# Kernel tuning notes

Hardware: AMD Instinct MI355X
Metric: run time of the kernel (lower is better)

The kernel has to match this reference:

```python
import jax, jax.numpy as jnp
import numpy as np

D_MODEL = 1024
NUM_HEADS = 16
HEAD_DIM = D_MODEL // NUM_HEADS


def setup_inputs() -> dict:
    key = jax.random.key(0)
    ks = jax.random.split(key, 10)
    B, L = 2, 2048
    s = 1.0 / np.sqrt(D_MODEL)
    x = jax.random.normal(ks[0], (B, L, D_MODEL), dtype=jnp.float32)
    Wq = jax.random.normal(ks[1], (D_MODEL, D_MODEL), dtype=jnp.float32) * s
    bq = jnp.zeros((D_MODEL,), dtype=jnp.float32)
    Wk = jax.random.normal(ks[2], (D_MODEL, D_MODEL), dtype=jnp.float32) * s
    bk = jnp.zeros((D_MODEL,), dtype=jnp.float32)
    Wv = jax.random.normal(ks[3], (D_MODEL, D_MODEL), dtype=jnp.float32) * s
    bv = jnp.zeros((D_MODEL,), dtype=jnp.float32)
    Wo = jax.random.normal(ks[4], (D_MODEL, D_MODEL), dtype=jnp.float32) * s
    bo = jnp.zeros((D_MODEL,), dtype=jnp.float32)
    # per-head retention decay; torch init is ones, use values near 1 for nontrivial decay
    gamma = jax.random.uniform(ks[5], (NUM_HEADS,), dtype=jnp.float32, minval=0.95, maxval=1.0)
    return {"x": x, "Wq": Wq, "bq": bq, "Wk": Wk, "bk": bk,
            "Wv": Wv, "bv": bv, "Wo": Wo, "bo": bo, "gamma": gamma}


def reference(x, Wq, bq, Wk, bk, Wv, bv, Wo, bo, gamma):
    B, L, D = x.shape
    H, hd = NUM_HEADS, HEAD_DIM
    # projections (torch Linear: x @ W.T + b), split heads -> [B, H, L, hd]
    q = (x @ Wq.T + bq).reshape(B, L, H, hd).transpose(0, 2, 1, 3)
    k = (x @ Wk.T + bk).reshape(B, L, H, hd).transpose(0, 2, 1, 3)
    v = (x @ Wv.T + bv).reshape(B, L, H, hd).transpose(0, 2, 1, 3)
    # per-head decay gamma_h^i applied along the query index (matches torch broadcast)
    idx = jnp.arange(L, dtype=x.dtype)
    decay = gamma[None, :, None, None] ** idx[None, None, :, None]  # [1, H, L, 1]
    scores = jnp.einsum('bhqd,bhkd->bhqk', q, k)  # [B, H, L, L]
    causal = jnp.tril(jnp.ones((L, L), dtype=x.dtype))
    scores = scores * causal[None, None] * decay
    out = jnp.einsum('bhqk,bhkd->bhqd', scores, v)  # [B, H, L, hd]
    out = out.transpose(0, 2, 1, 3).reshape(B, L, D)
    return out @ Wo.T + bo
```

## Files before the change

### kernel.cpp

```cpp
#include <hip/hip_runtime.h>
#include <hip/hip_bf16.h>

#define D_MODEL 1024
#define NUM_HEADS 16
#define HEAD_DIM 64
#define BATCH 2
#define SEQ 2048
#define M_TOT (BATCH*SEQ)
#define CHUNK 64
#define NCHUNK (SEQ/CHUNK)
#define LT 68

typedef __attribute__((ext_vector_type(8))) short bf16x8;
typedef __attribute__((ext_vector_type(8))) unsigned short us16x8;
typedef __attribute__((ext_vector_type(4))) float f32x4;

__device__ inline ushort f2bf(float f) {
    __hip_bfloat16 h = __float2bfloat16(f);
    return __builtin_bit_cast(ushort, h);
}

__device__ inline bf16x8 ld_frag(const ushort* p) {
    struct S { uint2 a, b; };
    S s;
    s.a = *(const uint2*)p;
    s.b = *(const uint2*)(p + 4);
    return __builtin_bit_cast(bf16x8, s);
}

__device__ inline void st16(ushort* dst, uint4 a, uint4 b) {
    *(uint2*)(dst + 0)  = make_uint2(a.x, a.y);
    *(uint2*)(dst + 4)  = make_uint2(a.z, a.w);
    *(uint2*)(dst + 8)  = make_uint2(b.x, b.y);
    *(uint2*)(dst + 12) = make_uint2(b.z, b.w);
}

__device__ inline void load_lds16(const ushort* g, ushort* l) {
    __builtin_amdgcn_global_load_lds(
        (const __attribute__((address_space(1))) unsigned int*)g,
        (__attribute__((address_space(3))) unsigned int*)l, 16, 0, 0);
}

#define XN (M_TOT * D_MODEL)
#define WN (D_MODEL * D_MODEL)
__global__ __launch_bounds__(256) void cast_all_kernel(const float* __restrict__ x,
                                                       const float* __restrict__ Wq,
                                                       const float* __restrict__ Wk,
                                                       const float* __restrict__ Wv,
                                                       const float* __restrict__ Wo,
                                                       ushort* __restrict__ dst) {
    size_t o = ((size_t)blockIdx.x * 256 + threadIdx.x) * 4;
    const float* src;
    if (o < XN)               src = x  + o;
    else if (o < XN + WN)     src = Wq + (o - XN);
    else if (o < XN + 2 * WN) src = Wk + (o - XN - WN);
    else if (o < XN + 3 * WN) src = Wv + (o - XN - 2 * (size_t)WN);
    else                      src = Wo + (o - XN - 3 * (size_t)WN);
    float4 f = *(const float4*)src;
    ushort4 u;
    u.x = f2bf(f.x); u.y = f2bf(f.y); u.z = f2bf(f.z); u.w = f2bf(f.w);
    *(ushort4*)(dst + o) = u;
}

__global__ __launch_bounds__(256) void decay_kernel(const float* __restrict__ gamma,
                                                    float* __restrict__ decay) {
    int idx = blockIdx.x * blockDim.x + threadIdx.x;
    if (idx < SEQ * NUM_HEADS) {
        int i = idx >> 4, h = idx & 15;
        decay[idx] = powf(gamma[h], (float)i);
    }
}

template <int NBUF, int OUT_BF16>
__global__ __launch_bounds__(256) void gemm128(const ushort* __restrict__ A,
                                               const ushort* __restrict__ Bt,
                                               const float* __restrict__ b0,
                                               const float* __restrict__ b1,
                                               const float* __restrict__ b2,
                                               void* __restrict__ o0,
                                               void* __restrict__ o1,
                                               void* __restrict__ o2,
                                               const float* __restrict__ decay) {
    const int K = 1024;
    __shared__ ushort lds_a[128 * 64];
    __shared__ ushort lds_b[128 * 64];
    int t = threadIdx.x;
    int lane = t & 63, w = t >> 6;
    int bm = blockIdx.y * 128, bn = blockIdx.x * 128;
    int wm = (w >> 1) * 64, wn = (w & 1) * 64;

    int lr = lane >> 3, lc = lane & 7;
    int gcol = lc ^ (lr & 7);
    const ushort* aBase = A  + (size_t)(bm + w * 32 + lr) * K + gcol * 8;
    const ushort* bBase = Bt + (size_t)(bn + w * 32 + lr) * K + gcol * 8;
    ushort* aLds = &lds_a[(w * 32) * 64];
    ushort* bLds = &lds_b[(w * 32) * 64];

    f32x4 acc[4][4];
    #pragma unroll
    for (int i = 0; i < 4; i++)
        #pragma unroll
        for (int j = 0; j < 4; j++)
            acc[i][j] = (f32x4){0.f, 0.f, 0.f, 0.f};

    int mrel = lane & 15, kq = lane >> 4;

    for (int k0 = 0; k0 < K; k0 += 64) {
        #pragma unroll
        for (int q = 0; q < 4; q++) {
            load_lds16(aBase + (size_t)q * 8 * K + k0, aLds + q * 512);
            load_lds16(bBase + (size_t)q * 8 * K + k0, bLds + q * 512);
        }
        __syncthreads();
        #pragma unroll
        for (int s = 0; s < 2; s++) {
            bf16x8 af[4], bfv[4];
            #pragma unroll
            for (int i = 0; i < 4; i++) {
                int row = wm + i * 16 + mrel;
                af[i] = ld_frag(&lds_a[row * 64 + (((s * 4 + kq) ^ (row & 7)) * 8)]);
            }
            #pragma unroll
            for (int j = 0; j < 4; j++) {
                int row = wn + j * 16 + mrel;
                bfv[j] = ld_frag(&lds_b[row * 64 + (((s * 4 + kq) ^ (row & 7)) * 8)]);
            }
            #pragma unroll
            for (int i = 0; i < 4; i++)
                #pragma unroll
                for (int j = 0; j < 4; j++)
                    acc[i][j] = __builtin_amdgcn_mfma_f32_16x16x32_bf16(af[i], bfv[j], acc[i][j], 0, 0, 0);
        }
        __syncthreads();
    }

    int quad = lane >> 4;
    int buf = (NBUF == 3) ? (bn >> 10) : 0;
    const float* bias = (buf == 0) ? b0 : (buf == 1) ? b1 : b2;
    void* dstv = (buf == 0) ? o0 : (buf == 1) ? o1 : o2;
    int cbase = ((NBUF == 3) ? (bn & 1023) : bn) + wn;
    #pragma unroll
    for (int j = 0; j < 4; j++) {
        int cl = cbase + j * 16 + mrel;
        float bv = bias[cl];
        #pragma unroll
        for (int i = 0; i < 4; i++) {
            #pragma unroll
            for (int reg = 0; reg < 4; reg++) {
                int row = bm + wm + i * 16 + quad * 4 + reg;
                float v = acc[i][j][reg] + bv;
                if (NBUF == 3 && buf == 0)
                    v *= decay[(row & (SEQ - 1)) * 16 + (cl >> 6)];
                if (OUT_BF16)
                    ((ushort*)dstv)[(size_t)row * 1024 + cl] = f2bf(v);
                else
                    ((float*)dstv)[(size_t)row * 1024 + cl] = v;
            }
        }
    }
}

__global__ __launch_bounds__(256) void chunk_kv_mfma(const ushort* __restrict__ kp,
                                                     const ushort* __restrict__ vp,
                                                     float* __restrict__ states) {
    __shared__ ushort Kt[64 * LT];
    __shared__ ushort Vt[64 * LT];
    int bx = blockIdx.x;
    int c = bx & 31, h = (bx >> 5) & 15, b = bx >> 9;
    int t = threadIdx.x, lane = t & 63, w = t >> 6;
    size_t rowbase = (size_t)(b * SEQ + c * 64);
    int r = t >> 2, cc = t & 3;
    const uint4* gk = (const uint4*)(kp + (rowbase + r) * D_MODEL + h * 64 + cc * 16);
    const uint4* gv = (const uint4*)(vp + (rowbase + r) * D_MODEL + h * 64 + cc * 16);
    uint4 k0 = gk[0], k1 = gk[1], v0 = gv[0], v1 = gv[1];
    {
        us16x8 ka = __builtin_bit_cast(us16x8, k0), kb = __builtin_bit_cast(us16x8, k1);
        us16x8 va = __builtin_bit_cast(us16x8, v0), vb = __builtin_bit_cast(us16x8, v1);
        #pragma unroll
        for (int i = 0; i < 8; i++) {
            Kt[(cc * 16 + i) * LT + r]     = ka[i];
            Kt[(cc * 16 + 8 + i) * LT + r] = kb[i];
            Vt[(cc * 16 + i) * LT + r]     = va[i];
            Vt[(cc * 16 + 8 + i) * LT + r] = vb[i];
        }
    }
    __syncthreads();
    int mrel = lane & 15, q8 = (lane >> 4) * 8, band = w * 16;
    bf16x8 af[2];
    af[0] = ld_frag(&Vt[(band + mrel) * LT + q8]);
    af[1] = ld_frag(&Vt[(band + mrel) * LT + 32 + q8]);
    f32x4 acc[4];
    #pragma unroll
    for (int dt = 0; dt < 4; dt++) acc[dt] = (f32x4){0.f, 0.f, 0.f, 0.f};
    #pragma unroll
    for (int dt = 0; dt < 4; dt++)
        #pragma unroll
        for (int kk = 0; kk < 2; kk++)
            acc[dt] = __builtin_amdgcn_mfma_f32_16x16x32_bf16(
                af[kk], ld_frag(&Kt[(dt * 16 + mrel) * LT + kk * 32 + q8]), acc[dt], 0, 0, 0);
    int quad = lane >> 4;
    float* sp = states + (size_t)bx * 4096;
    #pragma unroll
    for (int dt = 0; dt < 4; dt++)
        #pragma unroll
        for (int reg = 0; reg < 4; reg++)
            sp[(band + quad * 4 + reg) * 64 + dt * 16 + mrel] = acc[dt][reg];
}

__global__ __launch_bounds__(256) void prefix_kernel(const float* __restrict__ states,
                                                     ushort* __restrict__ statesb) {
    int bh = blockIdx.y;
    int e = blockIdx.x * 256 + threadIdx.x;
    const float* src = states + (size_t)bh * NCHUNK * 4096 + e;
    ushort* dst = statesb + (size_t)bh * NCHUNK * 4096 + e;
    float run = 0.f;
    for (int cb = 0; cb < NCHUNK; cb += 8) {
        float vals[8];
        #pragma unroll
        for (int u = 0; u < 8; u++) vals[u] = src[(size_t)(cb + u) * 4096];
        #pragma unroll
        for (int u = 0; u < 8; u++) {
            dst[(size_t)(cb + u) * 4096] = f2bf(run);
            run += vals[u];
        }
    }
}

__global__ __launch_bounds__(256) void attn_mfma(const ushort* __restrict__ qp,
                                                 const ushort* __restrict__ kp,
                                                 const ushort* __restrict__ vp,
                                                 const ushort* __restrict__ statesb,
                                                 ushort* __restrict__ attn_out) {
    __shared__ ushort Qs[64 * LT];
    __shared__ ushort Ks[64 * LT];
    __shared__ ushort Vt[64 * LT];
    __shared__ ushort St[64 * LT];
    __shared__ ushort Ps[64 * LT];
    int bx = blockIdx.x;
    int c = bx & 31, h = (bx >> 5) & 15, b = bx >> 9;
    int t = threadIdx.x, lane = t & 63, w = t >> 6;
    size_t rowbase = (size_t)(b * SEQ + c * 64);
    int r = t >> 2, cc = t & 3;
    {
        const uint4* gq = (const uint4*)(qp + (rowbase + r) * D_MODEL + h * 64 + cc * 16);
        const uint4* gk = (const uint4*)(kp + (rowbase + r) * D_MODEL + h * 64 + cc * 16);
        const uint4* gv = (const uint4*)(vp + (rowbase + r) * D_MODEL + h * 64 + cc * 16);
        const uint4* gs = (const uint4*)(statesb + (size_t)bx * 4096 + t * 16);
        uint4 q0 = gq[0], q1 = gq[1];
        uint4 k0 = gk[0], k1 = gk[1];
        uint4 v0 = gv[0], v1 = gv[1];
        uint4 s0 = gs[0], s1 = gs[1];
        st16(&Qs[r * LT + cc * 16], q0, q1);
        st16(&Ks[r * LT + cc * 16], k0, k1);
        st16(&St[r * LT + cc * 16], s0, s1);
        us16x8 va = __builtin_bit_cast(us16x8, v0), vb = __builtin_bit_cast(us16x8, v1);
        #pragma unroll
        for (int i = 0; i < 8; i++) {
            Vt[(cc * 16 + i) * LT + r]     = va[i];
            Vt[(cc * 16 + 8 + i) * LT + r] = vb[i];
        }
    }
    __syncthreads();

    int mrel = lane & 15, q8 = (lane >> 4) * 8, quad = lane >> 4, band = w * 16;
    bf16x8 af[2];
    af[0] = ld_frag(&Qs[(band + mrel) * LT + q8]);
    af[1] = ld_frag(&Qs[(band + mrel) * LT + 32 + q8]);

    f32x4 oacc[4];
    #pragma unroll
    for (int dt = 0; dt < 4; dt++) oacc[dt] = (f32x4){0.f, 0.f, 0.f, 0.f};
    #pragma unroll
    for (int dt = 0; dt < 4; dt++)
        #pragma unroll
        for (int kk = 0; kk < 2; kk++)
            oacc[dt] = __builtin_amdgcn_mfma_f32_16x16x32_bf16(
                af[kk], ld_frag(&St[(dt * 16 + mrel) * LT + kk * 32 + q8]), oacc[dt], 0, 0, 0);

    f32x4 pacc[4];
    #pragma unroll
    for (int jt = 0; jt < 4; jt++) pacc[jt] = (f32x4){0.f, 0.f, 0.f, 0.f};
    #pragma unroll
    for (int jt = 0; jt < 4; jt++) {
        if (jt <= w) {
            #pragma unroll
            for (int kk = 0; kk < 2; kk++)
                pacc[jt] = __builtin_amdgcn_mfma_f32_16x16x32_bf16(
                    af[kk], ld_frag(&Ks[(jt * 16 + mrel) * LT + kk * 32 + q8]), pacc[jt], 0, 0, 0);
        }
    }
    #pragma unroll
    for (int jt = 0; jt < 4; jt++) {
        #pragma unroll
        for (int reg = 0; reg < 4; reg++) {
            int i = band + quad * 4 + reg;
            int j = jt * 16 + mrel;
            float val = (jt <= w && j <= i) ? pacc[jt][reg] : 0.f;
            Ps[i * LT + j] = f2bf(val);
        }
    }
    __syncthreads();

    bf16x8 pf0 = ld_frag(&Ps[(band + mrel) * LT + q8]);
    #pragma unroll
    for (int dt = 0; dt < 4; dt++)
        oacc[dt] = __builtin_amdgcn_mfma_f32_16x16x32_bf16(
            pf0, ld_frag(&Vt[(dt * 16 + mrel) * LT + q8]), oacc[dt], 0, 0, 0);
    if (w >= 2) {
        bf16x8 pf1 = ld_frag(&Ps[(band + mrel) * LT + 32 + q8]);
        #pragma unroll
        for (int dt = 0; dt < 4; dt++)
            oacc[dt] = __builtin_amdgcn_mfma_f32_16x16x32_bf16(
                pf1, ld_frag(&Vt[(dt * 16 + mrel) * LT + 32 + q8]), oacc[dt], 0, 0, 0);
    }

    #pragma unroll
    for (int dt = 0; dt < 4; dt++) {
        #pragma unroll
        for (int reg = 0; reg < 4; reg++) {
            size_t row = rowbase + band + quad * 4 + reg;
            int col = h * 64 + dt * 16 + mrel;
            attn_out[row * D_MODEL + col] = f2bf(oacc[dt][reg]);
        }
    }
}

extern "C" void kernel_launch(void* const* d_in, const int* in_sizes, int n_in,
                              void* d_out, int out_size, void* d_ws, size_t ws_size,
                              hipStream_t stream) {
    (void)in_sizes; (void)n_in; (void)out_size; (void)ws_size;
    const float* x  = (const float*)d_in[0];
    const float* Wq = (const float*)d_in[1];
    const float* bq = (const float*)d_in[2];
    const float* Wk = (const float*)d_in[3];
    const float* bk = (const float*)d_in[4];
    const float* Wv = (const float*)d_in[5];
    const float* bv = (const float*)d_in[6];
    const float* Wo = (const float*)d_in[7];
    const float* bo = (const float*)d_in[8];
    const float* gamma = (const float*)d_in[9];
    float* out = (float*)d_out;

    uint8_t* w = (uint8_t*)d_ws;
    ushort* xb    = (ushort*)w; w += (size_t)XN * 2;
    ushort* wqkvb = (ushort*)w; w += (size_t)3 * WN * 2;
    ushort* wob   = (ushort*)w; w += (size_t)WN * 2;
    ushort* qb  = (ushort*)w; w += (size_t)XN * 2;
    ushort* kb  = (ushort*)w; w += (size_t)XN * 2;
    ushort* vb  = (ushort*)w; w += (size_t)XN * 2;
    float*  states  = (float*)w;  w += (size_t)BATCH * NUM_HEADS * NCHUNK * 4096 * 4;
    ushort* statesb = (ushort*)w; w += (size_t)BATCH * NUM_HEADS * NCHUNK * 4096 * 2;
    float*  decay   = (float*)w;  w += (size_t)SEQ * NUM_HEADS * 4;

    cast_all_kernel<<<(XN + 4 * WN) / 4 / 256, 256, 0, stream>>>(x, Wq, Wk, Wv, Wo, xb);
    decay_kernel<<<(SEQ * NUM_HEADS) / 256, 256, 0, stream>>>(gamma, decay);

    gemm128<3, 1><<<dim3(3072 / 128, M_TOT / 128), 256, 0, stream>>>(
        xb, wqkvb, bq, bk, bv, qb, kb, vb, decay);

    int nblk = BATCH * NUM_HEADS * NCHUNK;
    chunk_kv_mfma<<<nblk, 256, 0, stream>>>(kb, vb, states);
    prefix_kernel<<<dim3(16, 32), 256, 0, stream>>>(states, statesb);
    attn_mfma<<<nblk, 256, 0, stream>>>(qb, kb, vb, statesb, xb);

    gemm128<1, 0><<<dim3(1024 / 128, M_TOT / 128), 256, 0, stream>>>(
        xb, wob, bo, nullptr, nullptr, out, nullptr, nullptr, nullptr);
}
```

Measured before the change: 190.6 us.

## Fuse decay into cast kernel, remap GEMM blocks per XCD, store chunk states bf16

Computes the decay table inside the cast kernel using extra blocks, which removes one kernel launch. The GEMM block index is remapped so that blocks landing on the same XCD share columns of B, aiming for better L2 reuse. Chunk KV states are rounded to bf16 in LDS and written with coalesced 16-byte stores, and the prefix scan runs in place on the bf16 buffer, roughly halving state traffic. The in-place scan now sums values that were already rounded to bf16, so precision drops slightly.

```diff
diff --git a/kernel.cpp b/kernel.cpp
--- a/kernel.cpp
+++ b/kernel.cpp
@@ -19,6 +19,10 @@
     __hip_bfloat16 h = __float2bfloat16(f);
     return __builtin_bit_cast(ushort, h);
 }
+__device__ inline float bf2f(ushort u) {
+    unsigned int v = ((unsigned int)u) << 16;
+    return __builtin_bit_cast(float, v);
+}
 
 __device__ inline bf16x8 ld_frag(const ushort* p) {
     struct S { uint2 a, b; };
@@ -43,13 +47,23 @@
 
 #define XN (M_TOT * D_MODEL)
 #define WN (D_MODEL * D_MODEL)
+#define CAST_BLOCKS ((XN + 4 * WN) / 4 / 256)
 __global__ __launch_bounds__(256) void cast_all_kernel(const float* __restrict__ x,
                                                        const float* __restrict__ Wq,
                                                        const float* __restrict__ Wk,
                                                        const float* __restrict__ Wv,
                                                        const float* __restrict__ Wo,
-                                                       ushort* __restrict__ dst) {
-    size_t o = ((size_t)blockIdx.x * 256 + threadIdx.x) * 4;
+                                                       ushort* __restrict__ dst,
+                                                       const float* __restrict__ gamma,
+                                                       float* __restrict__ decay) {
+    int bx = blockIdx.x;
+    if (bx >= CAST_BLOCKS) {
+        int idx = (bx - CAST_BLOCKS) * 256 + threadIdx.x;
+        int i = idx >> 4, h = idx & 15;
+        decay[idx] = powf(gamma[h], (float)i);
+        return;
+    }
+    size_t o = ((size_t)bx * 256 + threadIdx.x) * 4;
     const float* src;
     if (o < XN)               src = x  + o;
     else if (o < XN + WN)     src = Wq + (o - XN);
@@ -60,15 +74,6 @@
     ushort4 u;
     u.x = f2bf(f.x); u.y = f2bf(f.y); u.z = f2bf(f.z); u.w = f2bf(f.w);
     *(ushort4*)(dst + o) = u;
-}
-
-__global__ __launch_bounds__(256) void decay_kernel(const float* __restrict__ gamma,
-                                                    float* __restrict__ decay) {
-    int idx = blockIdx.x * blockDim.x + threadIdx.x;
-    if (idx < SEQ * NUM_HEADS) {
-        int i = idx >> 4, h = idx & 15;
-        decay[idx] = powf(gamma[h], (float)i);
-    }
 }
 
 template <int NBUF, int OUT_BF16>
@@ -86,7 +91,12 @@
     __shared__ ushort lds_b[128 * 64];
     int t = threadIdx.x;
     int lane = t & 63, w = t >> 6;
-    int bm = blockIdx.y * 128, bn = blockIdx.x * 128;
+
+    int p = blockIdx.y * gridDim.x + blockIdx.x;
+    int xcd = p & 7, q = p >> 3;
+    int cpx = gridDim.x >> 3;
+    int bn = (xcd * cpx + (q % cpx)) * 128;
+    int bm = (q / cpx) * 128;
     int wm = (w >> 1) * 64, wn = (w & 1) * 64;
 
     int lr = lane >> 3, lc = lane & 7;
@@ -107,9 +117,9 @@
 
     for (int k0 = 0; k0 < K; k0 += 64) {
         #pragma unroll
-        for (int q = 0; q < 4; q++) {
-            load_lds16(aBase + (size_t)q * 8 * K + k0, aLds + q * 512);
-            load_lds16(bBase + (size_t)q * 8 * K + k0, bLds + q * 512);
+        for (int qq = 0; qq < 4; qq++) {
+            load_lds16(aBase + (size_t)qq * 8 * K + k0, aLds + qq * 512);
+            load_lds16(bBase + (size_t)qq * 8 * K + k0, bLds + qq * 512);
         }
         __syncthreads();
         #pragma unroll
@@ -162,7 +172,7 @@
 
 __global__ __launch_bounds__(256) void chunk_kv_mfma(const ushort* __restrict__ kp,
                                                      const ushort* __restrict__ vp,
-                                                     float* __restrict__ states) {
+                                                     ushort* __restrict__ statesb) {
     __shared__ ushort Kt[64 * LT];
     __shared__ ushort Vt[64 * LT];
     int bx = blockIdx.x;
@@ -185,7 +195,7 @@
         }
     }
     __syncthreads();
-    int mrel = lane & 15, q8 = (lane >> 4) * 8, band = w * 16;
+    int mrel = lane & 15, q8 = (lane >> 4) * 8, band = w * 16, quad = lane >> 4;
     bf16x8 af[2];
     af[0] = ld_frag(&Vt[(band + mrel) * LT + q8]);
     af[1] = ld_frag(&Vt[(band + mrel) * LT + 32 + q8]);
@@ -198,29 +208,34 @@
         for (int kk = 0; kk < 2; kk++)
             acc[dt] = __builtin_amdgcn_mfma_f32_16x16x32_bf16(
                 af[kk], ld_frag(&Kt[(dt * 16 + mrel) * LT + kk * 32 + q8]), acc[dt], 0, 0, 0);
-    int quad = lane >> 4;
-    float* sp = states + (size_t)bx * 4096;
+    __syncthreads();
     #pragma unroll
     for (int dt = 0; dt < 4; dt++)
         #pragma unroll
         for (int reg = 0; reg < 4; reg++)
-            sp[(band + quad * 4 + reg) * 64 + dt * 16 + mrel] = acc[dt][reg];
-}
-
-__global__ __launch_bounds__(256) void prefix_kernel(const float* __restrict__ states,
-                                                     ushort* __restrict__ statesb) {
+            Kt[(band + quad * 4 + reg) * LT + dt * 16 + mrel] = f2bf(acc[dt][reg]);
+    __syncthreads();
+    {
+        bf16x8 s0 = ld_frag(&Kt[r * LT + cc * 16]);
+        bf16x8 s1 = ld_frag(&Kt[r * LT + cc * 16 + 8]);
+        uint4* dst = (uint4*)(statesb + (size_t)bx * 4096 + r * 64 + cc * 16);
+        dst[0] = __builtin_bit_cast(uint4, s0);
+        dst[1] = __builtin_bit_cast(uint4, s1);
+    }
+}
+
+__global__ __launch_bounds__(256) void prefix_kernel(ushort* __restrict__ statesb) {
     int bh = blockIdx.y;
     int e = blockIdx.x * 256 + threadIdx.x;
-    const float* src = states + (size_t)bh * NCHUNK * 4096 + e;
-    ushort* dst = statesb + (size_t)bh * NCHUNK * 4096 + e;
+    ushort* p = statesb + (size_t)bh * NCHUNK * 4096 + e;
     float run = 0.f;
     for (int cb = 0; cb < NCHUNK; cb += 8) {
         float vals[8];
         #pragma unroll
-        for (int u = 0; u < 8; u++) vals[u] = src[(size_t)(cb + u) * 4096];
+        for (int u = 0; u < 8; u++) vals[u] = bf2f(p[(size_t)(cb + u) * 4096]);
         #pragma unroll
         for (int u = 0; u < 8; u++) {
-            dst[(size_t)(cb + u) * 4096] = f2bf(run);
+            p[(size_t)(cb + u) * 4096] = f2bf(run);
             run += vals[u];
         }
     }
@@ -348,19 +363,18 @@
     ushort* qb  = (ushort*)w; w += (size_t)XN * 2;
     ushort* kb  = (ushort*)w; w += (size_t)XN * 2;
     ushort* vb  = (ushort*)w; w += (size_t)XN * 2;
-    float*  states  = (float*)w;  w += (size_t)BATCH * NUM_HEADS * NCHUNK * 4096 * 4;
     ushort* statesb = (ushort*)w; w += (size_t)BATCH * NUM_HEADS * NCHUNK * 4096 * 2;
     float*  decay   = (float*)w;  w += (size_t)SEQ * NUM_HEADS * 4;
 
-    cast_all_kernel<<<(XN + 4 * WN) / 4 / 256, 256, 0, stream>>>(x, Wq, Wk, Wv, Wo, xb);
-    decay_kernel<<<(SEQ * NUM_HEADS) / 256, 256, 0, stream>>>(gamma, decay);
+    cast_all_kernel<<<CAST_BLOCKS + (SEQ * NUM_HEADS) / 256, 256, 0, stream>>>(
+        x, Wq, Wk, Wv, Wo, xb, gamma, decay);
 
     gemm128<3, 1><<<dim3(3072 / 128, M_TOT / 128), 256, 0, stream>>>(
         xb, wqkvb, bq, bk, bv, qb, kb, vb, decay);
 
     int nblk = BATCH * NUM_HEADS * NCHUNK;
-    chunk_kv_mfma<<<nblk, 256, 0, stream>>>(kb, vb, states);
-    prefix_kernel<<<dim3(16, 32), 256, 0, stream>>>(states, statesb);
+    chunk_kv_mfma<<<nblk, 256, 0, stream>>>(kb, vb, statesb);
+    prefix_kernel<<<dim3(16, 32), 256, 0, stream>>>(statesb);
     attn_mfma<<<nblk, 256, 0, stream>>>(qb, kb, vb, statesb, xb);
 
     gemm128<1, 0><<<dim3(1024 / 128, M_TOT / 128), 256, 0, stream>>>(
```

After: 193.6 us. No clear change (+1.5%).
